# Kernel tuning notes

Measured on AMD Instinct MI355X. Metric: run time of the kernel, lower is better.

## Reference

```python
import jax, jax.numpy as jnp
import numpy as np

HEADS = 12
EMBED = 768
HEAD_DIM = EMBED // HEADS


def setup_inputs() -> dict:
    key = jax.random.key(0)
    kx, kw, kb = jax.random.split(key, 3)
    x = jax.random.normal(kx, (8, 1024, EMBED), dtype=jnp.float32)
    # nn.Linear(embed, 3*embed): weight (3E, E), bias (3E,)
    W_qkv = jax.random.normal(kw, (3 * EMBED, EMBED), dtype=jnp.float32) * (1.0 / np.sqrt(EMBED))
    b_qkv = jax.random.normal(kb, (3 * EMBED,), dtype=jnp.float32) * 0.01
    return {"x": x, "W_qkv": W_qkv, "b_qkv": b_qkv}


def reference(x, W_qkv, b_qkv):
    b, n, e = x.shape
    qkv = x @ W_qkv.T + b_qkv                       # (b, n, 3E)
    qkv = qkv.reshape(b, n, HEADS, 3 * HEAD_DIM)    # (b, n, h, 3d)
    q, k, v = jnp.split(qkv, 3, axis=-1)            # each (b, n, h, d)
    scores = jnp.einsum('bihd,bjhd->bijh', q, k) / np.sqrt(HEAD_DIM)
    attn = jax.nn.softmax(scores, axis=-2)          # softmax over keys j (dim=-2)
    out = jnp.einsum('bijh,bjhd->bihd', attn, v)
    return out.reshape(b, n, e)
```

## Files before the change

### kernel.cpp

```cpp
#include <hip/hip_runtime.h>
#include <hip/hip_bf16.h>
#include <cstdint>

#define BATCH 8
#define SEQ   1024
#define EMB   768
#define HEADS 12
#define HDIM  64
#define C3    2304
#define MROWS (BATCH*SEQ)
#define KSLC  (EMB / 16)

typedef __attribute__((ext_vector_type(8)))  short bf16x8;
typedef __attribute__((ext_vector_type(4)))  short bf16x4;
typedef __attribute__((ext_vector_type(4)))  float f32x4;
typedef __attribute__((ext_vector_type(16))) float f32x16;

static __device__ inline short f2bf(float f) {
    union { float f; uint32_t u; } v; v.f = f;
    uint32_t u = v.u + 0x7fff + ((v.u >> 16) & 1);
    return (short)(u >> 16);
}

__global__ __launch_bounds__(256) void pack_bf16(const float* __restrict__ in,
                                                 short* __restrict__ out) {
    const int tid = blockIdx.x * 256 + threadIdx.x;
    const int r    = tid & 31;
    const int ks   = (tid >> 5) % KSLC;
    const int tile = tid / (KSLC * 32);
    const int row  = tile * 32 + r;

    const float* src = in + (size_t)row * EMB + ks * 16;
    float4 v0 = ((const float4*)src)[0];
    float4 v1 = ((const float4*)src)[1];
    float4 v2 = ((const float4*)src)[2];
    float4 v3 = ((const float4*)src)[3];
    bf16x8 o0 = { f2bf(v0.x), f2bf(v0.y), f2bf(v0.z), f2bf(v0.w),
                  f2bf(v1.x), f2bf(v1.y), f2bf(v1.z), f2bf(v1.w) };
    bf16x8 o1 = { f2bf(v2.x), f2bf(v2.y), f2bf(v2.z), f2bf(v2.w),
                  f2bf(v3.x), f2bf(v3.y), f2bf(v3.z), f2bf(v3.w) };
    short* dst = out + (size_t)tid * 16;
    *(bf16x8*)(dst)     = o0;
    *(bf16x8*)(dst + 8) = o1;
}

__global__ __launch_bounds__(256) void qkv_gemm_mfma(const short* __restrict__ xb2,
                                                     const short* __restrict__ Wb2,
                                                     const float* __restrict__ bias,
                                                     short* __restrict__ qkvb) {
    const int bx = blockIdx.x;
    const int by = blockIdx.y;
    const int t = threadIdx.x;
    const int w = t >> 6;
    const int lane = t & 63;
    const int l5  = lane >> 5;
    const int r31 = lane & 31;
    const int m0 = by * 128, n0 = bx * 128;
    const int wm = (w & 1) * 64, wn = (w >> 1) * 64;

    const int laneoff = r31 * 16 + l5 * 8;
    const short* pa0 = xb2 + ((size_t)((m0 + wm) >> 5) * KSLC) * 512 + laneoff;
    const short* pa1 = pa0 + (size_t)KSLC * 512;
    const short* pb0 = Wb2 + ((size_t)((n0 + wn) >> 5) * KSLC) * 512 + laneoff;
    const short* pb1 = pb0 + (size_t)KSLC * 512;

    f32x16 acc[2][2] = {};

    #pragma unroll 4
    for (int ks = 0; ks < KSLC; ++ks) {
        bf16x8 a0 = *(const bf16x8*)(pa0 + ks * 512);
        bf16x8 a1 = *(const bf16x8*)(pa1 + ks * 512);
        bf16x8 b0 = *(const bf16x8*)(pb0 + ks * 512);
        bf16x8 b1 = *(const bf16x8*)(pb1 + ks * 512);
        acc[0][0] = __builtin_amdgcn_mfma_f32_32x32x16_bf16(a0, b0, acc[0][0], 0, 0, 0);
        acc[0][1] = __builtin_amdgcn_mfma_f32_32x32x16_bf16(a0, b1, acc[0][1], 0, 0, 0);
        acc[1][0] = __builtin_amdgcn_mfma_f32_32x32x16_bf16(a1, b0, acc[1][0], 0, 0, 0);
        acc[1][1] = __builtin_amdgcn_mfma_f32_32x32x16_bf16(a1, b1, acc[1][1], 0, 0, 0);
    }

    float bsv[2], scl[2];
    #pragma unroll
    for (int nt = 0; nt < 2; ++nt) {
        int n = n0 + wn + nt * 32 + r31;
        bsv[nt] = bias[n];
        scl[nt] = ((n % 192) < 64) ? 0.125f : 1.0f;
    }
    #pragma unroll
    for (int mt = 0; mt < 2; ++mt)
        #pragma unroll
        for (int nt = 0; nt < 2; ++nt) {
            int n = n0 + wn + nt * 32 + r31;
            #pragma unroll
            for (int reg = 0; reg < 16; ++reg) {
                int row = (reg & 3) + 8 * (reg >> 2) + 4 * l5;
                int m = m0 + wm + mt * 32 + row;
                float v = (acc[mt][nt][reg] + bsv[nt]) * scl[nt];
                qkvb[(size_t)m * C3 + n] = f2bf(v);
            }
        }
}

__global__ __launch_bounds__(256) void v_transpose(const short* __restrict__ qkvb,
                                                   short* __restrict__ vt) {
    __shared__ int Lt[64][65];

    const int bh = blockIdx.x;
    const int jt = blockIdx.y;
    const int b = bh / HEADS, h = bh % HEADS;
    const int t = threadIdx.x;
    const int j0 = jt * 64;
    const size_t base = (size_t)b * SEQ * C3 + (size_t)h * 192 + 128;

    #pragma unroll
    for (int p = 0; p < 2; ++p) {
        int idx = p * 256 + t;
        int j = idx >> 3, d0 = (idx & 7) * 8;
        bf16x8 v = *(const bf16x8*)(qkvb + base + (size_t)(j0 + j) * C3 + d0);
        #pragma unroll
        for (int u = 0; u < 8; ++u)
            Lt[d0 + u][j] = (int)(unsigned short)v[u];
    }
    __syncthreads();
    #pragma unroll
    for (int p = 0; p < 2; ++p) {
        int idx = p * 256 + t;
        int d = idx >> 3, c8 = (idx & 7) * 8;
        bf16x8 o;
        #pragma unroll
        for (int u = 0; u < 8; ++u)
            o[u] = (short)Lt[d][c8 + u];
        *(bf16x8*)(vt + ((size_t)bh * 64 + d) * SEQ + j0 + c8) = o;
    }
}

#define LDP 72

__global__ __launch_bounds__(256, 3) void attn_mfma(const short* __restrict__ qkvb,
                                                    const short* __restrict__ vt,
                                                    float* __restrict__ out) {
    __shared__ short Ks[64][LDP];
    __shared__ short Vt[64][LDP];
    __shared__ short Ps[128][LDP];

    const int bx   = blockIdx.x;
    const int qt   = bx & 7;
    const int h    = (bx >> 3) % HEADS;
    const int b    = bx / (8 * HEADS);
    const int t    = threadIdx.x;
    const int w    = t >> 6;
    const int lane = t & 63;
    const int c    = lane & 15;
    const int q    = lane >> 4;
    const int i0   = qt * 128;

    const size_t base = (size_t)b * SEQ * C3 + (size_t)h * 192;
    const short* vtb = vt + (size_t)(b * HEADS + h) * 64 * SEQ;

    #pragma unroll
    for (int p = 0; p < 4; ++p) {
        int idx = p * 256 + t;
        int i = idx >> 3, d0 = (idx & 7) << 3;
        *(bf16x8*)&Ps[i][d0] =
            *(const bf16x8*)(qkvb + base + (size_t)(i0 + i) * C3 + d0);
    }
    __syncthreads();
    bf16x8 aq[2][2];
    #pragma unroll
    for (int s = 0; s < 2; ++s) {
        aq[s][0] = *(bf16x8*)&Ps[w * 32 + s * 16 + c][q * 8];
        aq[s][1] = *(bf16x8*)&Ps[w * 32 + s * 16 + c][32 + q * 8];
    }

    f32x4 o[2][4] = {};
    float l_acc[2] = {0.f, 0.f};

    for (int kt = 0; kt < 16; ++kt) {
        const int j0 = kt * 64;
        __syncthreads();
        #pragma unroll
        for (int p = 0; p < 2; ++p) {
            int idx = p * 256 + t;
            int j = idx >> 3, d0 = (idx & 7) << 3;
            *(bf16x8*)&Ks[j][d0] =
                *(const bf16x8*)(qkvb + base + 64 + (size_t)(j0 + j) * C3 + d0);
        }
        #pragma unroll
        for (int p = 0; p < 2; ++p) {
            int idx = p * 256 + t;
            int d = idx >> 3, j8 = (idx & 7) << 3;
            *(bf16x8*)&Vt[d][j8] =
                *(const bf16x8*)(vtb + (size_t)d * SEQ + j0 + j8);
        }
        __syncthreads();

        bf16x8 ka[4][2];
        #pragma unroll
        for (int mt = 0; mt < 4; ++mt) {
            ka[mt][0] = *(bf16x8*)&Ks[mt * 16 + c][q * 8];
            ka[mt][1] = *(bf16x8*)&Ks[mt * 16 + c][32 + q * 8];
        }

        f32x4 s[2][4];
        #pragma unroll
        for (int ss = 0; ss < 2; ++ss)
            #pragma unroll
            for (int mt = 0; mt < 4; ++mt) {
                f32x4 acc = {0.f, 0.f, 0.f, 0.f};
                acc = __builtin_amdgcn_mfma_f32_16x16x32_bf16(ka[mt][0], aq[ss][0], acc, 0, 0, 0);
                acc = __builtin_amdgcn_mfma_f32_16x16x32_bf16(ka[mt][1], aq[ss][1], acc, 0, 0, 0);
                s[ss][mt] = acc;
            }

        #pragma unroll
        for (int ss = 0; ss < 2; ++ss)
            #pragma unroll
            for (int mt = 0; mt < 4; ++mt) {
                float p0 = __expf(s[ss][mt][0]);
                float p1 = __expf(s[ss][mt][1]);
                float p2 = __expf(s[ss][mt][2]);
                float p3 = __expf(s[ss][mt][3]);
                l_acc[ss] += (p0 + p1) + (p2 + p3);
                bf16x4 pw = { f2bf(p0), f2bf(p1), f2bf(p2), f2bf(p3) };
                *(bf16x4*)&Ps[w * 32 + ss * 16 + c][mt * 16 + 4 * q] = pw;
            }

        bf16x8 vb[4][2];
        #pragma unroll
        for (int dt = 0; dt < 4; ++dt) {
            vb[dt][0] = *(bf16x8*)&Vt[dt * 16 + c][q * 8];
            vb[dt][1] = *(bf16x8*)&Vt[dt * 16 + c][32 + q * 8];
        }

        #pragma unroll
        for (int ss = 0; ss < 2; ++ss) {
            bf16x8 ap0 = *(bf16x8*)&Ps[w * 32 + ss * 16 + c][q * 8];
            bf16x8 ap1 = *(bf16x8*)&Ps[w * 32 + ss * 16 + c][32 + q * 8];
            #pragma unroll
            for (int dt = 0; dt < 4; ++dt) {
                o[ss][dt] = __builtin_amdgcn_mfma_f32_16x16x32_bf16(ap0, vb[dt][0], o[ss][dt], 0, 0, 0);
                o[ss][dt] = __builtin_amdgcn_mfma_f32_16x16x32_bf16(ap1, vb[dt][1], o[ss][dt], 0, 0, 0);
            }
        }
    }

    float linv[2][4];
    #pragma unroll
    for (int ss = 0; ss < 2; ++ss) {
        float v = l_acc[ss];
        v += __shfl_xor(v, 16, 64);
        v += __shfl_xor(v, 32, 64);
        #pragma unroll
        for (int r = 0; r < 4; ++r)
            linv[ss][r] = 1.0f / __shfl(v, 4 * q + r, 64);
    }

    #pragma unroll
    for (int ss = 0; ss < 2; ++ss)
        #pragma unroll
        for (int dt = 0; dt < 4; ++dt)
            #pragma unroll
            for (int r = 0; r < 4; ++r) {
                int i = w * 32 + ss * 16 + q * 4 + r;
                out[((size_t)b * SEQ + i0 + i) * EMB + h * HDIM + dt * 16 + c]
                    = o[ss][dt][r] * linv[ss][r];
            }
}

extern "C" void kernel_launch(void* const* d_in, const int* in_sizes, int n_in,
                              void* d_out, int out_size, void* d_ws, size_t ws_size,
                              hipStream_t stream) {
    const float* x    = (const float*)d_in[0];
    const float* W    = (const float*)d_in[1];
    const float* bias = (const float*)d_in[2];
    float* out = (float*)d_out;

    short* xb2  = (short*)d_ws;
    short* Wb2  = xb2 + (size_t)MROWS * EMB;
    short* qkvb = Wb2 + (size_t)C3 * EMB;
    short* vt   = qkvb + (size_t)MROWS * C3;

    pack_bf16<<<MROWS * KSLC / 256, 256, 0, stream>>>(x, xb2);
    pack_bf16<<<C3 * KSLC / 256, 256, 0, stream>>>(W, Wb2);

    dim3 g1(C3 / 128, MROWS / 128);
    qkv_gemm_mfma<<<g1, 256, 0, stream>>>(xb2, Wb2, bias, qkvb);

    dim3 g2(BATCH * HEADS, SEQ / 64);
    v_transpose<<<g2, 256, 0, stream>>>(qkvb, vt);

    attn_mfma<<<BATCH * HEADS * (SEQ / 128), 256, 0, stream>>>(qkvb, vt, out);
}
```

Measured before the change: 182.0 us.

## Merge pack launches and remap GEMM/attention block order for XCD L2 locality

The two fp32-to-bf16 pack launches are merged into one kernel that picks x or W by block index, removing one launch. The QKV GEMM switches to a 1D grid whose blocks are remapped so each XCD (blockIdx mod 8) works on a contiguous group of 8 M-tiles, which should improve L2 reuse of the x tiles. The attention grid is reordered so query tiles are the slow dimension. These index remappings change cache behaviour but leave the computed result the same.

```diff
diff --git a/kernel.cpp b/kernel.cpp
--- a/kernel.cpp
+++ b/kernel.cpp
@@ -10,6 +10,8 @@
 #define C3    2304
 #define MROWS (BATCH*SEQ)
 #define KSLC  (EMB / 16)
+#define XPACK_BLOCKS (MROWS * KSLC / 256)
+#define WPACK_BLOCKS (C3 * KSLC / 256)
 
 typedef __attribute__((ext_vector_type(8)))  short bf16x8;
 typedef __attribute__((ext_vector_type(4)))  short bf16x4;
@@ -22,9 +24,20 @@
     return (short)(u >> 16);
 }
 
-__global__ __launch_bounds__(256) void pack_bf16(const float* __restrict__ in,
-                                                 short* __restrict__ out) {
-    const int tid = blockIdx.x * 256 + threadIdx.x;
+__global__ __launch_bounds__(256) void pack_bf16(const float* __restrict__ x,
+                                                 short* __restrict__ xb2,
+                                                 const float* __restrict__ W,
+                                                 short* __restrict__ Wb2) {
+    const float* in;
+    short* out;
+    int tid;
+    if (blockIdx.x < XPACK_BLOCKS) {
+        in = x; out = xb2;
+        tid = blockIdx.x * 256 + threadIdx.x;
+    } else {
+        in = W; out = Wb2;
+        tid = (blockIdx.x - XPACK_BLOCKS) * 256 + threadIdx.x;
+    }
     const int r    = tid & 31;
     const int ks   = (tid >> 5) % KSLC;
     const int tile = tid / (KSLC * 32);
@@ -48,8 +61,12 @@
                                                      const short* __restrict__ Wb2,
                                                      const float* __restrict__ bias,
                                                      short* __restrict__ qkvb) {
-    const int bx = blockIdx.x;
-    const int by = blockIdx.y;
+    const int g    = blockIdx.x;
+    const int xcd  = g & 7;
+    const int ring = g >> 3;
+    const int by   = xcd * 8 + (ring & 7);
+    const int bx   = ring >> 3;
+
     const int t = threadIdx.x;
     const int w = t >> 6;
     const int lane = t & 63;
@@ -142,10 +159,11 @@
     __shared__ short Vt[64][LDP];
     __shared__ short Ps[128][LDP];
 
-    const int bx   = blockIdx.x;
-    const int qt   = bx & 7;
-    const int h    = (bx >> 3) % HEADS;
-    const int b    = bx / (8 * HEADS);
+    const int g    = blockIdx.x;
+    const int qt   = g / (BATCH * HEADS);
+    const int bh   = g % (BATCH * HEADS);
+    const int b    = bh / HEADS;
+    const int h    = bh % HEADS;
     const int t    = threadIdx.x;
     const int w    = t >> 6;
     const int lane = t & 63;
@@ -154,7 +172,7 @@
     const int i0   = qt * 128;
 
     const size_t base = (size_t)b * SEQ * C3 + (size_t)h * 192;
-    const short* vtb = vt + (size_t)(b * HEADS + h) * 64 * SEQ;
+    const short* vtb = vt + (size_t)bh * 64 * SEQ;
 
     #pragma unroll
     for (int p = 0; p < 4; ++p) {
@@ -279,11 +297,9 @@
     short* qkvb = Wb2 + (size_t)C3 * EMB;
     short* vt   = qkvb + (size_t)MROWS * C3;
 
-    pack_bf16<<<MROWS * KSLC / 256, 256, 0, stream>>>(x, xb2);
-    pack_bf16<<<C3 * KSLC / 256, 256, 0, stream>>>(W, Wb2);
-
-    dim3 g1(C3 / 128, MROWS / 128);
-    qkv_gemm_mfma<<<g1, 256, 0, stream>>>(xb2, Wb2, bias, qkvb);
+    pack_bf16<<<XPACK_BLOCKS + WPACK_BLOCKS, 256, 0, stream>>>(x, xb2, W, Wb2);
+
+    qkv_gemm_mfma<<<1152, 256, 0, stream>>>(xb2, Wb2, bias, qkvb);
 
     dim3 g2(BATCH * HEADS, SEQ / 64);
     v_transpose<<<g2, 256, 0, stream>>>(qkvb, vt);
```

Measured after the change: 171.1 us. -6.0%, faster.
